# Performance work log

Hardware: AMD Instinct MI355X
Metric: run time of the kernel (lower is better)

Reference implementation:

```python
import jax, jax.numpy as jnp
import numpy as np

N = 131072   # total utterances (nodes)
B = 2048     # conversations (segments)
F = 200      # n_features (hard-coded 200 in source)
STEPS = 3    # processing_steps (reason_steps[0])


def setup_inputs() -> dict:
    key = jax.random.key(0)
    k = jax.random.split(key, 8)
    x = jax.random.normal(k[0], (N, F), dtype=jnp.float32)
    batch = jnp.sort(jax.random.randint(k[1], (N,), 0, B, dtype=jnp.int32))
    cos_coef = jax.random.normal(k[2], (N,), dtype=jnp.float32)
    q_star = jax.random.normal(k[3], (B, 2 * F), dtype=jnp.float32)
    s = 1.0 / np.sqrt(F)
    # PyTorch LSTM params: gate order i, f, g, o; input size 2F, hidden F
    W_ih = jax.random.uniform(k[4], (4 * F, 2 * F), jnp.float32, -s, s)
    W_hh = jax.random.uniform(k[5], (4 * F, F), jnp.float32, -s, s)
    b_ih = jax.random.uniform(k[6], (4 * F,), jnp.float32, -s, s)
    b_hh = jax.random.uniform(k[7], (4 * F,), jnp.float32, -s, s)
    return {"x": x, "batch": batch, "cos_coef": cos_coef, "q_star": q_star,
            "W_ih": W_ih, "W_hh": W_hh, "b_ih": b_ih, "b_hh": b_hh}


def _lstm_cell(inp, h, c, W_ih, W_hh, b_ih, b_hh):
    gates = inp @ W_ih.T + b_ih + h @ W_hh.T + b_hh  # [B, 4F]
    i, f, g, o = jnp.split(gates, 4, axis=-1)
    c = jax.nn.sigmoid(f) * c + jax.nn.sigmoid(i) * jnp.tanh(g)
    h = jax.nn.sigmoid(o) * jnp.tanh(c)
    return h, c


def reference(x, batch, cos_coef, q_star, W_ih, W_hh, b_ih, b_hh):
    # initial LSTM hidden: a_sit[i] = cos_row_i @ x[segment_i]  -> segment_sum
    h = jax.ops.segment_sum(cos_coef[:, None] * x, batch, num_segments=B)  # [B,F]
    c = jnp.zeros((B, F), dtype=x.dtype)
    for _ in range(STEPS):
        h, c = _lstm_cell(q_star, h, c, W_ih, W_hh, b_ih, b_hh)
        q = h                                            # [B,F]
        e = jnp.sum(x * q[batch], axis=-1)               # [N]
        m = jax.ops.segment_max(e, batch, num_segments=B)
        ex = jnp.exp(e - m[batch])
        denom = jax.ops.segment_sum(ex, batch, num_segments=B)
        a = ex / denom[batch]                            # per-segment softmax
        r = jax.ops.segment_sum(a[:, None] * x, batch, num_segments=B)  # [B,F]
        q_star = jnp.concatenate([q, r], axis=-1)        # [B,2F]
    return q_star
```

## Files before the change

### kernel.cpp

```cpp
#include <hip/hip_runtime.h>
#include <hip/hip_bf16.h>

#define N_NODES 131072
#define B_SEG   2048
#define F_DIM   200
#define K_DIM   608
#define NEG_INF (-3.4e38f)

typedef __attribute__((ext_vector_type(8))) short bf16x8;
typedef __attribute__((ext_vector_type(4))) float f32x4;

__device__ __forceinline__ float b2f(unsigned short u) {
  union { unsigned int i; float f; } v; v.i = ((unsigned int)u) << 16; return v.f;
}
__device__ __forceinline__ unsigned short f2bu(float f) {
  __hip_bfloat16 h = __float2bfloat16(f);
  return *reinterpret_cast<unsigned short*>(&h);
}
__device__ __forceinline__ float sigmoidf_(float x) { return 1.f / (1.f + __expf(-x)); }

__global__ __launch_bounds__(256) void setup_kernel(
    const float* __restrict__ Wih, const float* __restrict__ Whh,
    const float* __restrict__ bih, const float* __restrict__ bhh,
    const int* __restrict__ batch, unsigned short* __restrict__ Wc,
    float* __restrict__ bsum, int* __restrict__ seg_off) {
  int bid = blockIdx.x, tid = threadIdx.x;
  if (bid < 1976) {
    int idx = bid * 256 + tid;
    int row = idx / K_DIM, k = idx - row * K_DIM;
    float v = 0.f;
    if (row < 800) {
      if (k < 400)      v = Wih[row * 400 + k];
      else if (k < 600) v = Whh[row * 200 + (k - 400)];
    }
    Wc[idx] = f2bu(v);
  } else if (bid < 1976 + 512) {
    int i = (bid - 1976) * 256 + tid;
    int v  = batch[i];
    int pv = (i == 0) ? -1 : batch[i - 1];
    for (int b = pv + 1; b <= v; b++) seg_off[b] = i;
  } else {
    int idx = (bid - 2488) * 256 + tid;
    if (idx < 800) bsum[idx] = bih[idx] + bhh[idx];
    else if (idx == 800) {
      int last = batch[N_NODES - 1];
      for (int b = last + 1; b <= B_SEG; b++) seg_off[b] = N_NODES;
    }
  }
}

__global__ __launch_bounds__(256) void init_kernel(
    const float* __restrict__ xf, const int* __restrict__ seg_off,
    const float* __restrict__ cosc, const float* __restrict__ qs0,
    unsigned short* __restrict__ xb, unsigned short* __restrict__ A) {
  __shared__ float rpart[5][F_DIM];
  int b = blockIdx.x, tid = threadIdx.x;
  int start = seg_off[b], end = seg_off[b + 1];
  int n = end - start;
  unsigned short* Arow = A + (size_t)b * K_DIM;
  int rgrp = tid / 50, col4 = tid - rgrp * 50;
  float a0 = 0.f, a1 = 0.f, a2 = 0.f, a3 = 0.f;
  if (rgrp < 5) {
    for (int r = rgrp; r < n; r += 5) {
      float4 v = *(const float4*)(xf + (size_t)(start + r) * F_DIM + 4 * col4);
      ushort4 o; o.x = f2bu(v.x); o.y = f2bu(v.y); o.z = f2bu(v.z); o.w = f2bu(v.w);
      *(ushort4*)(xb + (size_t)(start + r) * F_DIM + 4 * col4) = o;
      float cv = cosc[start + r];
      a0 += cv * b2f(o.x); a1 += cv * b2f(o.y);
      a2 += cv * b2f(o.z); a3 += cv * b2f(o.w);
    }
    rpart[rgrp][4 * col4]     = a0;
    rpart[rgrp][4 * col4 + 1] = a1;
    rpart[rgrp][4 * col4 + 2] = a2;
    rpart[rgrp][4 * col4 + 3] = a3;
  }
  if (tid < 100) {
    float4 v = *(const float4*)(qs0 + (size_t)b * 400 + 4 * tid);
    ushort4 o; o.x = f2bu(v.x); o.y = f2bu(v.y); o.z = f2bu(v.z); o.w = f2bu(v.w);
    *(ushort4*)(Arow + 4 * tid) = o;
  }
  if (tid < 8) Arow[600 + tid] = 0;
  __syncthreads();
  if (tid < F_DIM) {
    float acc = rpart[0][tid] + rpart[1][tid] + rpart[2][tid] + rpart[3][tid]
              + rpart[4][tid];
    Arow[400 + tid] = f2bu(acc);
  }
}

__global__ __launch_bounds__(256) void gemm_gates(
    const unsigned short* __restrict__ A, const unsigned short* __restrict__ W,
    float* __restrict__ gates) {
  int tid = threadIdx.x;
  int bm = blockIdx.x * 32, bn = blockIdx.y * 64;
  int wave = tid >> 6, lane = tid & 63;
  int quad = lane >> 4, col = lane & 15;
  int strip = wave >> 1;
  int tp = (wave & 1) * 2;
  f32x4 acc[2];
  acc[0] = (f32x4){0.f, 0.f, 0.f, 0.f};
  acc[1] = (f32x4){0.f, 0.f, 0.f, 0.f};
  const unsigned short* Ap = A + (size_t)(bm + strip * 16 + col) * K_DIM + quad * 8;
  const unsigned short* Wp = W + (size_t)(bn + col) * K_DIM + quad * 8;
#pragma unroll
  for (int k0 = 0; k0 < K_DIM; k0 += 32) {
    bf16x8 af = *(const bf16x8*)(Ap + k0);
#pragma unroll
    for (int t = 0; t < 2; t++) {
      bf16x8 bfr = *(const bf16x8*)(Wp + (size_t)(tp + t) * 16 * K_DIM + k0);
      acc[t] = __builtin_amdgcn_mfma_f32_16x16x32_bf16(af, bfr, acc[t], 0, 0, 0);
    }
  }
#pragma unroll
  for (int t = 0; t < 2; t++) {
    int gn = bn + (tp + t) * 16 + col;
    if (gn < 800) {
#pragma unroll
      for (int r = 0; r < 4; r++) {
        int gm = bm + strip * 16 + quad * 4 + r;
        gates[(size_t)gm * 800 + gn] = acc[t][r];
      }
    }
  }
}

__global__ __launch_bounds__(256) void attn_fused(
    const unsigned short* __restrict__ xb, const int* __restrict__ seg_off,
    const float* __restrict__ gates, const float* __restrict__ bsum,
    float* __restrict__ cvec, unsigned short* __restrict__ A,
    float* __restrict__ out, int step) {
  __shared__ float q_s[F_DIM];
  __shared__ float rpart[8][F_DIM];
  __shared__ float redm[8], redl[8];
  int b = blockIdx.x, tid = threadIdx.x;
  int start = seg_off[b], end = seg_off[b + 1];
  int n = end - start;
  unsigned short* Arow = A + (size_t)b * K_DIM;
  if (tid < F_DIM) {
    int f = tid;
    const float* g = gates + (size_t)b * 800;
    float gi = g[f]       + bsum[f];
    float gf = g[200 + f] + bsum[200 + f];
    float gg = g[400 + f] + bsum[400 + f];
    float go = g[600 + f] + bsum[600 + f];
    float cp = (step > 0) ? cvec[(size_t)b * F_DIM + f] : 0.f;
    float cn = sigmoidf_(gf) * cp + sigmoidf_(gi) * tanhf(gg);
    float hn = sigmoidf_(go) * tanhf(cn);
    cvec[(size_t)b * F_DIM + f] = cn;
    q_s[f] = hn;
    if (step < 2) {
      unsigned short hb = f2bu(hn);
      Arow[f] = hb;
      Arow[400 + f] = hb;
    }
  }
  __syncthreads();
  int wave = tid >> 6, lane = tid & 63;
  int half = lane >> 5, hl = lane & 31;
  int hw = wave * 2 + half;
  bool act = (hl < 25);
  float q0=0,q1=0,q2=0,q3=0,q4=0,q5=0,q6=0,q7=0;
  if (act) {
    q0 = q_s[8*hl];   q1 = q_s[8*hl+1]; q2 = q_s[8*hl+2]; q3 = q_s[8*hl+3];
    q4 = q_s[8*hl+4]; q5 = q_s[8*hl+5]; q6 = q_s[8*hl+6]; q7 = q_s[8*hl+7];
  }
  const unsigned short* xp = xb + (size_t)start * F_DIM + 8 * hl;
  float m = NEG_INF, l = 0.f;
  float a0=0,a1=0,a2=0,a3=0,a4=0,a5=0,a6=0,a7=0;
  for (int r = hw; r < n; r += 8) {
    float x0=0,x1=0,x2=0,x3=0,x4=0,x5=0,x6=0,x7=0;
    float p = 0.f;
    if (act) {
      uint4 v = *(const uint4*)(xp + (size_t)r * F_DIM);
      x0 = b2f((unsigned short)(v.x & 0xffff)); x1 = b2f((unsigned short)(v.x >> 16));
      x2 = b2f((unsigned short)(v.y & 0xffff)); x3 = b2f((unsigned short)(v.y >> 16));
      x4 = b2f((unsigned short)(v.z & 0xffff)); x5 = b2f((unsigned short)(v.z >> 16));
      x6 = b2f((unsigned short)(v.w & 0xffff)); x7 = b2f((unsigned short)(v.w >> 16));
      p = q0*x0 + q1*x1 + q2*x2 + q3*x3 + q4*x4 + q5*x5 + q6*x6 + q7*x7;
    }
#pragma unroll
    for (int off = 16; off; off >>= 1) p += __shfl_xor(p, off, 32);
    float e = p;
    float mn = fmaxf(m, e);
    float fac = __expf(m - mn);
    float w  = __expf(e - mn);
    l  = l * fac + w;
    a0 = a0*fac + w*x0; a1 = a1*fac + w*x1; a2 = a2*fac + w*x2; a3 = a3*fac + w*x3;
    a4 = a4*fac + w*x4; a5 = a5*fac + w*x5; a6 = a6*fac + w*x6; a7 = a7*fac + w*x7;
    m = mn;
  }
  if (hl == 0) redm[hw] = m;
  __syncthreads();
  float M = fmaxf(fmaxf(fmaxf(redm[0], redm[1]), fmaxf(redm[2], redm[3])),
                  fmaxf(fmaxf(redm[4], redm[5]), fmaxf(redm[6], redm[7])));
  float facw = (m > NEG_INF) ? __expf(m - M) : 0.f;
  if (hl == 0) redl[hw] = l * facw;
  if (act) {
    float* rp = &rpart[hw][8 * hl];
    rp[0] = a0*facw; rp[1] = a1*facw; rp[2] = a2*facw; rp[3] = a3*facw;
    rp[4] = a4*facw; rp[5] = a5*facw; rp[6] = a6*facw; rp[7] = a7*facw;
  }
  __syncthreads();
  float L = redl[0]+redl[1]+redl[2]+redl[3]+redl[4]+redl[5]+redl[6]+redl[7];
  float inv = (L > 0.f) ? 1.f / L : 0.f;
  if (tid < F_DIM) {
    float rv = (rpart[0][tid]+rpart[1][tid]+rpart[2][tid]+rpart[3][tid]
              + rpart[4][tid]+rpart[5][tid]+rpart[6][tid]+rpart[7][tid]) * inv;
    if (step < 2) {
      Arow[200 + tid] = f2bu(rv);
    } else {
      out[(size_t)b * 400 + tid]       = q_s[tid];
      out[(size_t)b * 400 + 200 + tid] = rv;
    }
  }
}

extern "C" void kernel_launch(void* const* d_in, const int* in_sizes, int n_in,
                              void* d_out, int out_size, void* d_ws, size_t ws_size,
                              hipStream_t stream) {
  const float* x    = (const float*)d_in[0];
  const int*   batch= (const int*)d_in[1];
  const float* cosc = (const float*)d_in[2];
  const float* qs0  = (const float*)d_in[3];
  const float* Wih  = (const float*)d_in[4];
  const float* Whh  = (const float*)d_in[5];
  const float* bih  = (const float*)d_in[6];
  const float* bhh  = (const float*)d_in[7];
  char* ws = (char*)d_ws;
  unsigned short* xb   = (unsigned short*)(ws);
  unsigned short* A    = (unsigned short*)(ws + 52428800);
  unsigned short* Wc   = (unsigned short*)(ws + 54919168);
  float*          gates= (float*)(ws + 55930880);
  float*          cvec = (float*)(ws + 62484480);
  float*          bsum = (float*)(ws + 64122880);
  int*            soff = (int*)(ws + 64126080);
  float*          outp = (float*)d_out;

  setup_kernel<<<2492, 256, 0, stream>>>(Wih, Whh, bih, bhh, batch, Wc, bsum, soff);
  init_kernel<<<B_SEG, 256, 0, stream>>>(x, soff, cosc, qs0, xb, A);
  for (int s = 0; s < 3; s++) {
    gemm_gates<<<dim3(64, 13), 256, 0, stream>>>(A, Wc, gates);
    attn_fused<<<B_SEG, 256, 0, stream>>>(xb, soff, gates, bsum, cvec, A, outp, s);
  }
}
```

Before: 273.9 us.

## Fuse setup into init kernel, binary-search segments, prefetch rows, fast tanh

Merges setup_kernel into init_kernel, so each block finds its segment bounds by binary search over the sorted batch array and also converts part of the weight matrix to bf16. This drops one launch and the serial dependency on seg_off. The attention loop now software-prefetches the next x row into registers, and tanhf is replaced with an exp-based approximation. The tradeoffs are extra binary-search loads per block, higher register pressure, and possible precision or overflow issues in tanh for large inputs.

```diff
diff --git a/kernel.cpp b/kernel.cpp
--- a/kernel.cpp
+++ b/kernel.cpp
@@ -18,15 +18,33 @@
   return *reinterpret_cast<unsigned short*>(&h);
 }
 __device__ __forceinline__ float sigmoidf_(float x) { return 1.f / (1.f + __expf(-x)); }
-
-__global__ __launch_bounds__(256) void setup_kernel(
+__device__ __forceinline__ float tanhf_(float x) {
+  float e = __expf(2.f * x);
+  return 1.f - 2.f / (1.f + e);
+}
+__device__ __forceinline__ int lower_bound_batch(const int* __restrict__ batch, int target) {
+  int lo = 0, hi = N_NODES;
+  while (lo < hi) {
+    int mid = (lo + hi) >> 1;
+    if (batch[mid] < target) lo = mid + 1; else hi = mid;
+  }
+  return lo;
+}
+
+__global__ __launch_bounds__(256) void init_kernel(
+    const float* __restrict__ xf, const int* __restrict__ batch,
+    const float* __restrict__ cosc, const float* __restrict__ qs0,
     const float* __restrict__ Wih, const float* __restrict__ Whh,
     const float* __restrict__ bih, const float* __restrict__ bhh,
-    const int* __restrict__ batch, unsigned short* __restrict__ Wc,
-    float* __restrict__ bsum, int* __restrict__ seg_off) {
-  int bid = blockIdx.x, tid = threadIdx.x;
-  if (bid < 1976) {
-    int idx = bid * 256 + tid;
+    unsigned short* __restrict__ xb, unsigned short* __restrict__ A,
+    unsigned short* __restrict__ Wc, float* __restrict__ bsum,
+    int* __restrict__ seg_off) {
+  __shared__ float rpart[5][F_DIM];
+  __shared__ int sb[2];
+  int b = blockIdx.x, tid = threadIdx.x;
+  if (tid < 2) sb[tid] = lower_bound_batch(batch, b + tid);
+  int idx = b * 256 + tid;
+  if (idx < 832 * K_DIM) {
     int row = idx / K_DIM, k = idx - row * K_DIM;
     float v = 0.f;
     if (row < 800) {
@@ -34,29 +52,15 @@
       else if (k < 600) v = Whh[row * 200 + (k - 400)];
     }
     Wc[idx] = f2bu(v);
-  } else if (bid < 1976 + 512) {
-    int i = (bid - 1976) * 256 + tid;
-    int v  = batch[i];
-    int pv = (i == 0) ? -1 : batch[i - 1];
-    for (int b = pv + 1; b <= v; b++) seg_off[b] = i;
-  } else {
-    int idx = (bid - 2488) * 256 + tid;
-    if (idx < 800) bsum[idx] = bih[idx] + bhh[idx];
-    else if (idx == 800) {
-      int last = batch[N_NODES - 1];
-      for (int b = last + 1; b <= B_SEG; b++) seg_off[b] = N_NODES;
-    }
-  }
-}
-
-__global__ __launch_bounds__(256) void init_kernel(
-    const float* __restrict__ xf, const int* __restrict__ seg_off,
-    const float* __restrict__ cosc, const float* __restrict__ qs0,
-    unsigned short* __restrict__ xb, unsigned short* __restrict__ A) {
-  __shared__ float rpart[5][F_DIM];
-  int b = blockIdx.x, tid = threadIdx.x;
-  int start = seg_off[b], end = seg_off[b + 1];
+  }
+  if (idx < 800) bsum[idx] = bih[idx] + bhh[idx];
+  __syncthreads();
+  int start = sb[0], end = sb[1];
   int n = end - start;
+  if (tid == 0) {
+    seg_off[b] = start;
+    if (b == 0) seg_off[B_SEG] = N_NODES;
+  }
   unsigned short* Arow = A + (size_t)b * K_DIM;
   int rgrp = tid / 50, col4 = tid - rgrp * 50;
   float a0 = 0.f, a1 = 0.f, a2 = 0.f, a3 = 0.f;
@@ -144,8 +148,8 @@
     float gg = g[400 + f] + bsum[400 + f];
     float go = g[600 + f] + bsum[600 + f];
     float cp = (step > 0) ? cvec[(size_t)b * F_DIM + f] : 0.f;
-    float cn = sigmoidf_(gf) * cp + sigmoidf_(gi) * tanhf(gg);
-    float hn = sigmoidf_(go) * tanhf(cn);
+    float cn = sigmoidf_(gf) * cp + sigmoidf_(gi) * tanhf_(gg);
+    float hn = sigmoidf_(go) * tanhf_(cn);
     cvec[(size_t)b * F_DIM + f] = cn;
     q_s[f] = hn;
     if (step < 2) {
@@ -167,17 +171,18 @@
   const unsigned short* xp = xb + (size_t)start * F_DIM + 8 * hl;
   float m = NEG_INF, l = 0.f;
   float a0=0,a1=0,a2=0,a3=0,a4=0,a5=0,a6=0,a7=0;
-  for (int r = hw; r < n; r += 8) {
-    float x0=0,x1=0,x2=0,x3=0,x4=0,x5=0,x6=0,x7=0;
-    float p = 0.f;
-    if (act) {
-      uint4 v = *(const uint4*)(xp + (size_t)r * F_DIM);
-      x0 = b2f((unsigned short)(v.x & 0xffff)); x1 = b2f((unsigned short)(v.x >> 16));
-      x2 = b2f((unsigned short)(v.y & 0xffff)); x3 = b2f((unsigned short)(v.y >> 16));
-      x4 = b2f((unsigned short)(v.z & 0xffff)); x5 = b2f((unsigned short)(v.z >> 16));
-      x6 = b2f((unsigned short)(v.w & 0xffff)); x7 = b2f((unsigned short)(v.w >> 16));
-      p = q0*x0 + q1*x1 + q2*x2 + q3*x3 + q4*x4 + q5*x5 + q6*x6 + q7*x7;
-    }
+  int r = hw;
+  uint4 v = {0u, 0u, 0u, 0u};
+  if (act && r < n) v = *(const uint4*)(xp + (size_t)r * F_DIM);
+  for (; r < n; r += 8) {
+    uint4 vc = v;
+    int rn = r + 8;
+    if (act && rn < n) v = *(const uint4*)(xp + (size_t)rn * F_DIM);
+    float x0 = b2f((unsigned short)(vc.x & 0xffff)), x1 = b2f((unsigned short)(vc.x >> 16));
+    float x2 = b2f((unsigned short)(vc.y & 0xffff)), x3 = b2f((unsigned short)(vc.y >> 16));
+    float x4 = b2f((unsigned short)(vc.z & 0xffff)), x5 = b2f((unsigned short)(vc.z >> 16));
+    float x6 = b2f((unsigned short)(vc.w & 0xffff)), x7 = b2f((unsigned short)(vc.w >> 16));
+    float p = act ? (q0*x0 + q1*x1 + q2*x2 + q3*x3 + q4*x4 + q5*x5 + q6*x6 + q7*x7) : 0.f;
 #pragma unroll
     for (int off = 16; off; off >>= 1) p += __shfl_xor(p, off, 32);
     float e = p;
@@ -236,8 +241,8 @@
   int*            soff = (int*)(ws + 64126080);
   float*          outp = (float*)d_out;
 
-  setup_kernel<<<2492, 256, 0, stream>>>(Wih, Whh, bih, bhh, batch, Wc, bsum, soff);
-  init_kernel<<<B_SEG, 256, 0, stream>>>(x, soff, cosc, qs0, xb, A);
+  init_kernel<<<B_SEG, 256, 0, stream>>>(x, batch, cosc, qs0, Wih, Whh, bih, bhh,
+                                         xb, A, Wc, bsum, soff);
   for (int s = 0; s < 3; s++) {
     gemm_gates<<<dim3(64, 13), 256, 0, stream>>>(A, Wc, gates);
     attn_fused<<<B_SEG, 256, 0, stream>>>(xb, soff, gates, bsum, cvec, A, outp, s);
```

Measured after the change: 274.0 us. No clear change (+0.0%).
